# Kernel optimization log

Hardware: AMD Instinct MI355X
Metric: run time of the kernel (lower is better)

Reference implementation:

```python
import jax, jax.numpy as jnp
import numpy as np

B, L, D, F, T = 32, 768, 256, 256, 3072
_EPS = 1e-5


def _layernorm(h, g, b):
    mu = jnp.mean(h, axis=-1, keepdims=True)
    var = jnp.var(h, axis=-1, keepdims=True)
    return (h - mu) * jax.lax.rsqrt(var + _EPS) * g + b


def _conv1d(h, w, b):
    # h: [B, L, Cin], w: [K, Cin, Cout] (HIO), padding=1 matches torch Conv1d(padding=1)
    return jax.lax.conv_general_dilated(h, w, (1,), [(1, 1)], dimension_numbers=('NHC', 'HIO', 'NHC')) + b


def setup_inputs() -> dict:
    key = jax.random.key(0)
    ks = jax.random.split(key, 6)
    return {
        'x': jax.random.normal(ks[0], (B, L, D), jnp.float32),
        'target': jax.random.randint(ks[1], (B, L), 0, 4, jnp.int32),
        'mel_max_length': T,
        'conv1_w': jax.random.normal(ks[2], (3, D, F), jnp.float32) * 0.05,
        'conv1_b': jnp.zeros((F,), jnp.float32),
        'ln1_g': jnp.ones((F,), jnp.float32),
        'ln1_b': jnp.zeros((F,), jnp.float32),
        'conv2_w': jax.random.normal(ks[3], (3, F, F), jnp.float32) * 0.05,
        'conv2_b': jnp.zeros((F,), jnp.float32),
        'ln2_g': jnp.ones((F,), jnp.float32),
        'ln2_b': jnp.zeros((F,), jnp.float32),
        'lin_w': jax.random.normal(ks[4], (F, 1), jnp.float32) * 0.05,
        'lin_b': jnp.zeros((1,), jnp.float32),
    }


def reference(x, target, mel_max_length, conv1_w, conv1_b, ln1_g, ln1_b,
              conv2_w, conv2_b, ln2_g, ln2_b, lin_w, lin_b):
    alpha = 1.0
    # DurationPredictor: conv -> relu -> LN -> conv -> relu -> LN -> linear (dropout=0)
    h = _layernorm(jax.nn.relu(_conv1d(x, conv1_w, conv1_b)), ln1_g, ln1_b)
    h = _layernorm(jax.nn.relu(_conv1d(h, conv2_w, conv2_b)), ln2_g, ln2_b)
    dp_out = (h @ lin_w + lin_b)[..., 0]                       # [B, L]
    durations = jnp.exp(dp_out) * alpha                        # [B, L] float
    # Training branch: durations come from target
    dpo = jnp.round(target.astype(jnp.float32) * alpha).astype(jnp.int32)  # [B, L]
    # LR: alignment @ x realized as cumulative-duration searchsorted + gather
    cum = jnp.cumsum(dpo, axis=1)                              # [B, L]
    t = jnp.arange(mel_max_length, dtype=jnp.int32)            # [T]
    idx = jax.vmap(lambda c: jnp.searchsorted(c, t, side='right'))(cum)  # [B, T]
    mask = (t[None, :] < cum[:, -1:]).astype(x.dtype)          # [B, T] zero past total frames
    out = jnp.take_along_axis(x, jnp.clip(idx, 0, x.shape[1] - 1)[:, :, None], axis=1)
    out = out * mask[:, :, None]                               # [B, T, D]
    return (out, dpo, durations)
```

## Files before the change

### kernel.cpp

```cpp
#include <hip/hip_runtime.h>
#include <hip/hip_bf16.h>
#include <math.h>

#define BB 32
#define LL 768
#define DD 256
#define FF 256
#define TT 3072
#define MT 48
#define PAD 262
#define A1R 66

typedef __attribute__((ext_vector_type(8))) short bf16x8;
typedef __attribute__((ext_vector_type(4))) float f32x4;

__device__ inline unsigned short f2b(float f) {
    union { float f; unsigned u; } v; v.f = f;
    unsigned r = (v.u + 0x7FFF + ((v.u >> 16) & 1)) >> 16;
    return (unsigned short)r;
}

#define DPP_ROR_ADD(v, ctrl)                                                   \
    v += __int_as_float(__builtin_amdgcn_update_dpp(                           \
        0, __float_as_int(v), ctrl, 0xF, 0xF, false))

__device__ inline void red16_pair(float& a, float& b) {
    DPP_ROR_ADD(a, 0x128); DPP_ROR_ADD(b, 0x128);
    DPP_ROR_ADD(a, 0x124); DPP_ROR_ADD(b, 0x124);
    DPP_ROR_ADD(a, 0x122); DPP_ROR_ADD(b, 0x122);
    DPP_ROR_ADD(a, 0x121); DPP_ROR_ADD(b, 0x121);
}

__device__ inline float red16_one(float a) {
    DPP_ROR_ADD(a, 0x128);
    DPP_ROR_ADD(a, 0x124);
    DPP_ROR_ADD(a, 0x122);
    DPP_ROR_ADD(a, 0x121);
    return a;
}

__global__ __launch_bounds__(256) void prep_w_kernel(
    const float* __restrict__ w1, const float* __restrict__ w2,
    unsigned short* __restrict__ wQ1, unsigned short* __restrict__ wQ2)
{
    const int layer = blockIdx.x / 24;
    const int s  = blockIdx.x % 24;
    const int kc = s >> 3, c8 = s & 7;
    const float* __restrict__ w = layer ? w2 : w1;
    unsigned short* __restrict__ o = (layer ? wQ2 : wQ1) + s * 8192 + threadIdx.x * 32;
    const int n = threadIdx.x;

    alignas(16) unsigned short tmp[32];
#pragma unroll
    for (int q = 0; q < 4; ++q)
#pragma unroll
        for (int j = 0; j < 8; ++j) {
            const int cin = c8 * 32 + q * 8 + j;
            tmp[q * 8 + j] = f2b(w[((size_t)(kc * 256 + cin)) * 256 + n]);
        }
#pragma unroll
    for (int i = 0; i < 4; ++i)
        *reinterpret_cast<uint4*>(o + i * 8) = *reinterpret_cast<const uint4*>(tmp + i * 8);
}

__global__ __launch_bounds__(256) void fused_dp_kernel(
    const float* __restrict__ x,
    const unsigned short* __restrict__ wQ1,
    const unsigned short* __restrict__ wQ2,
    const float* __restrict__ c1b, const float* __restrict__ g1, const float* __restrict__ b1,
    const float* __restrict__ c2b, const float* __restrict__ g2, const float* __restrict__ b2,
    const float* __restrict__ lw,  const float* __restrict__ lb,
    float* __restrict__ out_dur)
{
    __shared__ union {
        unsigned short A1[A1R * PAD];
        unsigned short h2[50 * PAD];
    } sm;
    __shared__ float red[4][4][4][4][2];
    __shared__ float redp[4][3][4][4];
    __shared__ float fin[50][2];

    const int tid  = threadIdx.x;
    const int b    = blockIdx.x / (LL / MT);
    const int l0   = (blockIdx.x % (LL / MT)) * MT;
    const int wave = tid >> 6, lane = tid & 63;
    const int quad = lane >> 4, l16 = lane & 15;

    int   cols[4];
    float c1bv[4], g1v[4], b1v[4], c2bv[4], g2v[4], b2v[4], lwv[4];
#pragma unroll
    for (int nt = 0; nt < 4; ++nt) {
        const int c = wave * 64 + nt * 16 + l16;
        cols[nt] = c;
        c1bv[nt] = c1b[c]; g1v[nt] = g1[c]; b1v[nt] = b1[c];
        c2bv[nt] = c2b[c]; g2v[nt] = g2[c]; b2v[nt] = b2[c];
        lwv[nt]  = lw[c];
    }
    const float lbv = lb[0];

    {
        const int ch = (tid & 31) * 8;
        const int rr = tid >> 5;
        for (int p = 0; p < 9; ++p) {
            const int ar = p * 8 + rr;
            if (ar >= A1R) break;
            const int l = l0 - 2 + ar;
            bf16x8 val;
#pragma unroll
            for (int j = 0; j < 8; ++j) val[j] = 0;
            if (ar < 52 && l >= 0 && l < LL) {
                const float* pp = x + ((size_t)b * LL + l) * DD + ch;
                const float4 v0 = *reinterpret_cast<const float4*>(pp);
                const float4 v1 = *reinterpret_cast<const float4*>(pp + 4);
                val[0] = (short)f2b(v0.x); val[1] = (short)f2b(v0.y);
                val[2] = (short)f2b(v0.z); val[3] = (short)f2b(v0.w);
                val[4] = (short)f2b(v1.x); val[5] = (short)f2b(v1.y);
                val[6] = (short)f2b(v1.z); val[7] = (short)f2b(v1.w);
            }
            *reinterpret_cast<bf16x8*>(&sm.A1[ar * PAD + ch]) = val;
        }
    }
    __syncthreads();

    f32x4 acc1[4][4] = {};
    for (int s = 0; s < 24; ++s) {
        const int kc = s >> 3, c8 = s & 7;
        bf16x8 a[4], bf[4];
#pragma unroll
        for (int mt = 0; mt < 4; ++mt)
            a[mt] = *reinterpret_cast<const bf16x8*>(
                &sm.A1[(16 * mt + l16 + kc) * PAD + c8 * 32 + quad * 8]);
#pragma unroll
        for (int nt = 0; nt < 4; ++nt)
            bf[nt] = *reinterpret_cast<const bf16x8*>(
                wQ1 + (size_t)s * 8192 + cols[nt] * 32 + quad * 8);
#pragma unroll
        for (int mt = 0; mt < 4; ++mt)
#pragma unroll
            for (int nt = 0; nt < 4; ++nt)
                acc1[mt][nt] = __builtin_amdgcn_mfma_f32_16x16x32_bf16(
                    a[mt], bf[nt], acc1[mt][nt], 0, 0, 0);
    }
    __syncthreads();

#pragma unroll
    for (int mt = 0; mt < 4; ++mt)
#pragma unroll
        for (int r = 0; r < 4; ++r) {
            float s1 = 0.f, s2 = 0.f;
#pragma unroll
            for (int nt = 0; nt < 4; ++nt) {
                const float v = fmaxf(acc1[mt][nt][r] + c1bv[nt], 0.f);
                s1 += v; s2 += v * v;
            }
            red16_pair(s1, s2);
            if (l16 == 0) { red[wave][mt][quad][r][0] = s1; red[wave][mt][quad][r][1] = s2; }
        }
    __syncthreads();
    if (tid < 50) {
        const int mt = tid >> 4, q = (tid >> 2) & 3, r = tid & 3;
        const float s1 = red[0][mt][q][r][0] + red[1][mt][q][r][0]
                       + red[2][mt][q][r][0] + red[3][mt][q][r][0];
        const float s2 = red[0][mt][q][r][1] + red[1][mt][q][r][1]
                       + red[2][mt][q][r][1] + red[3][mt][q][r][1];
        const float mu  = s1 * (1.f / 256.f);
        const float var = s2 * (1.f / 256.f) - mu * mu;
        fin[tid][0] = mu;
        fin[tid][1] = rsqrtf(var + 1e-5f);
    }
    __syncthreads();

#pragma unroll
    for (int mt = 0; mt < 4; ++mt)
#pragma unroll
        for (int r = 0; r < 4; ++r) {
            const int rho = 16 * mt + quad * 4 + r;
            if (rho < 50) {
                const int gr = l0 - 1 + rho;
                const float mu = fin[rho][0], rstd = fin[rho][1];
#pragma unroll
                for (int nt = 0; nt < 4; ++nt) {
                    unsigned short hv = 0;
                    if (gr >= 0 && gr < LL) {
                        const float v = fmaxf(acc1[mt][nt][r] + c1bv[nt], 0.f);
                        hv = f2b((v - mu) * rstd * g1v[nt] + b1v[nt]);
                    }
                    sm.h2[rho * PAD + cols[nt]] = hv;
                }
            }
        }
    __syncthreads();

    f32x4 acc2[3][4] = {};
    for (int s = 0; s < 24; ++s) {
        const int kc = s >> 3, c8 = s & 7;
        bf16x8 a[3], bf[4];
#pragma unroll
        for (int mt = 0; mt < 3; ++mt)
            a[mt] = *reinterpret_cast<const bf16x8*>(
                &sm.h2[(16 * mt + l16 + kc) * PAD + c8 * 32 + quad * 8]);
#pragma unroll
        for (int nt = 0; nt < 4; ++nt)
            bf[nt] = *reinterpret_cast<const bf16x8*>(
                wQ2 + (size_t)s * 8192 + cols[nt] * 32 + quad * 8);
#pragma unroll
        for (int mt = 0; mt < 3; ++mt)
#pragma unroll
            for (int nt = 0; nt < 4; ++nt)
                acc2[mt][nt] = __builtin_amdgcn_mfma_f32_16x16x32_bf16(
                    a[mt], bf[nt], acc2[mt][nt], 0, 0, 0);
    }

#pragma unroll
    for (int mt = 0; mt < 3; ++mt)
#pragma unroll
        for (int r = 0; r < 4; ++r) {
            float s1 = 0.f, s2 = 0.f;
#pragma unroll
            for (int nt = 0; nt < 4; ++nt) {
                const float v = fmaxf(acc2[mt][nt][r] + c2bv[nt], 0.f);
                s1 += v; s2 += v * v;
            }
            red16_pair(s1, s2);
            if (l16 == 0) { red[wave][mt][quad][r][0] = s1; red[wave][mt][quad][r][1] = s2; }
        }
    __syncthreads();
    if (tid < MT) {
        const int mt = tid >> 4, q = (tid >> 2) & 3, r = tid & 3;
        const float s1 = red[0][mt][q][r][0] + red[1][mt][q][r][0]
                       + red[2][mt][q][r][0] + red[3][mt][q][r][0];
        const float s2 = red[0][mt][q][r][1] + red[1][mt][q][r][1]
                       + red[2][mt][q][r][1] + red[3][mt][q][r][1];
        const float mu  = s1 * (1.f / 256.f);
        const float var = s2 * (1.f / 256.f) - mu * mu;
        fin[tid][0] = mu;
        fin[tid][1] = rsqrtf(var + 1e-5f);
    }
    __syncthreads();

#pragma unroll
    for (int mt = 0; mt < 3; ++mt)
#pragma unroll
        for (int r = 0; r < 4; ++r) {
            const int rho = 16 * mt + quad * 4 + r;
            const float mu = fin[rho][0], rstd = fin[rho][1];
            float p = 0.f;
#pragma unroll
            for (int nt = 0; nt < 4; ++nt) {
                const float v = fmaxf(acc2[mt][nt][r] + c2bv[nt], 0.f);
                p += ((v - mu) * rstd * g2v[nt] + b2v[nt]) * lwv[nt];
            }
            p = red16_one(p);
            if (l16 == 0) redp[wave][mt][quad][r] = p;
        }
    __syncthreads();
    if (tid < MT) {
        const int mt = tid >> 4, q = (tid >> 2) & 3, r = tid & 3;
        const float dp = redp[0][mt][q][r] + redp[1][mt][q][r]
                       + redp[2][mt][q][r] + redp[3][mt][q][r] + lbv;
        out_dur[(size_t)b * LL + l0 + tid] = expf(dp);
    }
}

__global__ __launch_bounds__(256) void scan_kernel(
    const int* __restrict__ target,
    float* __restrict__ out_dpo,
    int* __restrict__ idx_map)
{
    __shared__ int tsum[256];
    const int b = blockIdx.x, tid = threadIdx.x;

    const int l = 3 * tid;
    const int v0 = target[b * LL + l];
    const int v1 = target[b * LL + l + 1];
    const int v2 = target[b * LL + l + 2];
    out_dpo[b * LL + l]     = (float)v0;
    out_dpo[b * LL + l + 1] = (float)v1;
    out_dpo[b * LL + l + 2] = (float)v2;

    const int s0 = v0, s1 = v0 + v1, s2 = v0 + v1 + v2;
    tsum[tid] = s2;
    __syncthreads();
    for (int off = 1; off < 256; off <<= 1) {
        int xq = (tid >= off) ? tsum[tid - off] : 0;
        __syncthreads();
        tsum[tid] += xq;
        __syncthreads();
    }
    const int excl = tsum[tid] - s2;

    for (int t = tid; t < TT; t += 256) idx_map[b * TT + t] = -1;
    __syncthreads();

    const int c0 = excl + s0, c1 = excl + s1, c2 = excl + s2;
    for (int t = excl; t < c0 && t < TT; ++t) idx_map[b * TT + t] = l;
    for (int t = c0;   t < c1 && t < TT; ++t) idx_map[b * TT + t] = l + 1;
    for (int t = c1;   t < c2 && t < TT; ++t) idx_map[b * TT + t] = l + 2;
}

__global__ __launch_bounds__(256) void gather_kernel(
    const float* __restrict__ x,
    const int* __restrict__ idx_map,
    float* __restrict__ out)
{
    const int wv = threadIdx.x >> 6, lane = threadIdx.x & 63;
    const int row = blockIdx.x * 4 + wv;
    const int b = row / TT, t = row - b * TT;
    const int idx = idx_map[b * TT + t];
    f32x4 val = {0.f, 0.f, 0.f, 0.f};
    if (idx >= 0)
        val = *reinterpret_cast<const f32x4*>(x + ((size_t)(b * LL + idx)) * DD + lane * 4);
    __builtin_nontemporal_store(val, reinterpret_cast<f32x4*>(out) + (size_t)row * (DD / 4) + lane);
}

extern "C" void kernel_launch(void* const* d_in, const int* in_sizes, int n_in,
                              void* d_out, int out_size, void* d_ws, size_t ws_size,
                              hipStream_t stream)
{
    const float* x      = (const float*)d_in[0];
    const int*   target = (const int*)  d_in[1];
    const float* c1w = (const float*)d_in[3];
    const float* c1b = (const float*)d_in[4];
    const float* g1  = (const float*)d_in[5];
    const float* b1  = (const float*)d_in[6];
    const float* c2w = (const float*)d_in[7];
    const float* c2b = (const float*)d_in[8];
    const float* g2  = (const float*)d_in[9];
    const float* b2  = (const float*)d_in[10];
    const float* lw  = (const float*)d_in[11];
    const float* lb  = (const float*)d_in[12];

    float* out0    = (float*)d_out;
    float* out_dpo = out0 + (size_t)BB * TT * DD;
    float* out_dur = out_dpo + (size_t)BB * LL;

    char* ws = (char*)d_ws;
    unsigned short* wQ1 = (unsigned short*)ws;                 ws += (size_t)24 * 8192 * 2;
    unsigned short* wQ2 = (unsigned short*)ws;                 ws += (size_t)24 * 8192 * 2;
    int* idx_map        = (int*)ws;

    prep_w_kernel<<<48, 256, 0, stream>>>(c1w, c2w, wQ1, wQ2);

    fused_dp_kernel<<<BB * (LL / MT), 256, 0, stream>>>(
        x, wQ1, wQ2, c1b, g1, b1, c2b, g2, b2, lw, lb, out_dur);

    scan_kernel<<<BB, 256, 0, stream>>>(target, out_dpo, idx_map);
    gather_kernel<<<BB * TT / 4, 256, 0, stream>>>(x, idx_map, out0);
}
```

Baseline: 199.4 us.

## Merge weight prep with scan kernel and widen fused conv block to 8 waves

```diff
diff --git a/kernel.cpp b/kernel.cpp
--- a/kernel.cpp
+++ b/kernel.cpp
@@ -39,31 +39,69 @@
     return a;
 }
 
-__global__ __launch_bounds__(256) void prep_w_kernel(
+__global__ __launch_bounds__(256) void prep_scan_kernel(
     const float* __restrict__ w1, const float* __restrict__ w2,
-    unsigned short* __restrict__ wQ1, unsigned short* __restrict__ wQ2)
+    unsigned short* __restrict__ wQ1, unsigned short* __restrict__ wQ2,
+    const int* __restrict__ target,
+    float* __restrict__ out_dpo,
+    int* __restrict__ idx_map)
 {
-    const int layer = blockIdx.x / 24;
-    const int s  = blockIdx.x % 24;
-    const int kc = s >> 3, c8 = s & 7;
-    const float* __restrict__ w = layer ? w2 : w1;
-    unsigned short* __restrict__ o = (layer ? wQ2 : wQ1) + s * 8192 + threadIdx.x * 32;
-    const int n = threadIdx.x;
-
-    alignas(16) unsigned short tmp[32];
-#pragma unroll
-    for (int q = 0; q < 4; ++q)
-#pragma unroll
-        for (int j = 0; j < 8; ++j) {
-            const int cin = c8 * 32 + q * 8 + j;
-            tmp[q * 8 + j] = f2b(w[((size_t)(kc * 256 + cin)) * 256 + n]);
-        }
-#pragma unroll
-    for (int i = 0; i < 4; ++i)
-        *reinterpret_cast<uint4*>(o + i * 8) = *reinterpret_cast<const uint4*>(tmp + i * 8);
-}
-
-__global__ __launch_bounds__(256) void fused_dp_kernel(
+    __shared__ int tsum[256];
+    const int tid = threadIdx.x;
+
+    if (blockIdx.x < 48) {
+        const int layer = blockIdx.x / 24;
+        const int s  = blockIdx.x % 24;
+        const int kc = s >> 3, c8 = s & 7;
+        const float* __restrict__ w = layer ? w2 : w1;
+        unsigned short* __restrict__ o = (layer ? wQ2 : wQ1) + s * 8192 + tid * 32;
+        const int n = tid;
+
+        alignas(16) unsigned short tmp[32];
+#pragma unroll
+        for (int q = 0; q < 4; ++q)
+#pragma unroll
+            for (int j = 0; j < 8; ++j) {
+                const int cin = c8 * 32 + q * 8 + j;
+                tmp[q * 8 + j] = f2b(w[((size_t)(kc * 256 + cin)) * 256 + n]);
+            }
+#pragma unroll
+        for (int i = 0; i < 4; ++i)
+            *reinterpret_cast<uint4*>(o + i * 8) = *reinterpret_cast<const uint4*>(tmp + i * 8);
+        return;
+    }
+
+    const int b = blockIdx.x - 48;
+
+    const int l = 3 * tid;
+    const int v0 = target[b * LL + l];
+    const int v1 = target[b * LL + l + 1];
+    const int v2 = target[b * LL + l + 2];
+    out_dpo[b * LL + l]     = (float)v0;
+    out_dpo[b * LL + l + 1] = (float)v1;
+    out_dpo[b * LL + l + 2] = (float)v2;
+
+    const int s0 = v0, s1 = v0 + v1, s2 = v0 + v1 + v2;
+    tsum[tid] = s2;
+    __syncthreads();
+    for (int off = 1; off < 256; off <<= 1) {
+        int xq = (tid >= off) ? tsum[tid - off] : 0;
+        __syncthreads();
+        tsum[tid] += xq;
+        __syncthreads();
+    }
+    const int excl = tsum[tid] - s2;
+
+    for (int t = tid; t < TT; t += 256) idx_map[b * TT + t] = -1;
+    __syncthreads();
+
+    const int c0 = excl + s0, c1 = excl + s1, c2 = excl + s2;
+    for (int t = excl; t < c0 && t < TT; ++t) idx_map[b * TT + t] = l;
+    for (int t = c0;   t < c1 && t < TT; ++t) idx_map[b * TT + t] = l + 1;
+    for (int t = c1;   t < c2 && t < TT; ++t) idx_map[b * TT + t] = l + 2;
+}
+
+__global__ __launch_bounds__(512, 4) void fused_dp_kernel(
     const float* __restrict__ x,
     const unsigned short* __restrict__ wQ1,
     const unsigned short* __restrict__ wQ2,
@@ -76,8 +114,8 @@
         unsigned short A1[A1R * PAD];
         unsigned short h2[50 * PAD];
     } sm;
-    __shared__ float red[4][4][4][4][2];
-    __shared__ float redp[4][3][4][4];
+    __shared__ float red[8][4][4][4][2];
+    __shared__ float redp[8][3][4][4];
     __shared__ float fin[50][2];
 
     const int tid  = threadIdx.x;
@@ -86,11 +124,11 @@
     const int wave = tid >> 6, lane = tid & 63;
     const int quad = lane >> 4, l16 = lane & 15;
 
-    int   cols[4];
-    float c1bv[4], g1v[4], b1v[4], c2bv[4], g2v[4], b2v[4], lwv[4];
-#pragma unroll
-    for (int nt = 0; nt < 4; ++nt) {
-        const int c = wave * 64 + nt * 16 + l16;
+    int   cols[2];
+    float c1bv[2], g1v[2], b1v[2], c2bv[2], g2v[2], b2v[2], lwv[2];
+#pragma unroll
+    for (int nt = 0; nt < 2; ++nt) {
+        const int c = wave * 32 + nt * 16 + l16;
         cols[nt] = c;
         c1bv[nt] = c1b[c]; g1v[nt] = g1[c]; b1v[nt] = b1[c];
         c2bv[nt] = c2b[c]; g2v[nt] = g2[c]; b2v[nt] = b2[c];
@@ -101,8 +139,8 @@
     {
         const int ch = (tid & 31) * 8;
         const int rr = tid >> 5;
-        for (int p = 0; p < 9; ++p) {
-            const int ar = p * 8 + rr;
+        for (int p = 0; p < 5; ++p) {
+            const int ar = p * 16 + rr;
             if (ar >= A1R) break;
             const int l = l0 - 2 + ar;
             bf16x8 val;
@@ -122,22 +160,22 @@
     }
     __syncthreads();
 
-    f32x4 acc1[4][4] = {};
+    f32x4 acc1[4][2] = {};
     for (int s = 0; s < 24; ++s) {
         const int kc = s >> 3, c8 = s & 7;
-        bf16x8 a[4], bf[4];
+        bf16x8 a[4], bf[2];
 #pragma unroll
         for (int mt = 0; mt < 4; ++mt)
             a[mt] = *reinterpret_cast<const bf16x8*>(
                 &sm.A1[(16 * mt + l16 + kc) * PAD + c8 * 32 + quad * 8]);
 #pragma unroll
-        for (int nt = 0; nt < 4; ++nt)
+        for (int nt = 0; nt < 2; ++nt)
             bf[nt] = *reinterpret_cast<const bf16x8*>(
                 wQ1 + (size_t)s * 8192 + cols[nt] * 32 + quad * 8);
 #pragma unroll
         for (int mt = 0; mt < 4; ++mt)
 #pragma unroll
-            for (int nt = 0; nt < 4; ++nt)
+            for (int nt = 0; nt < 2; ++nt)
                 acc1[mt][nt] = __builtin_amdgcn_mfma_f32_16x16x32_bf16(
                     a[mt], bf[nt], acc1[mt][nt], 0, 0, 0);
     }
@@ -149,7 +187,7 @@
         for (int r = 0; r < 4; ++r) {
             float s1 = 0.f, s2 = 0.f;
 #pragma unroll
-            for (int nt = 0; nt < 4; ++nt) {
+            for (int nt = 0; nt < 2; ++nt) {
                 const float v = fmaxf(acc1[mt][nt][r] + c1bv[nt], 0.f);
                 s1 += v; s2 += v * v;
             }
@@ -159,10 +197,9 @@
     __syncthreads();
     if (tid < 50) {
         const int mt = tid >> 4, q = (tid >> 2) & 3, r = tid & 3;
-        const float s1 = red[0][mt][q][r][0] + red[1][mt][q][r][0]
-                       + red[2][mt][q][r][0] + red[3][mt][q][r][0];
-        const float s2 = red[0][mt][q][r][1] + red[1][mt][q][r][1]
-                       + red[2][mt][q][r][1] + red[3][mt][q][r][1];
+        float s1 = 0.f, s2 = 0.f;
+#pragma unroll
+        for (int w = 0; w < 8; ++w) { s1 += red[w][mt][q][r][0]; s2 += red[w][mt][q][r][1]; }
         const float mu  = s1 * (1.f / 256.f);
         const float var = s2 * (1.f / 256.f) - mu * mu;
         fin[tid][0] = mu;
@@ -179,7 +216,7 @@
                 const int gr = l0 - 1 + rho;
                 const float mu = fin[rho][0], rstd = fin[rho][1];
 #pragma unroll
-                for (int nt = 0; nt < 4; ++nt) {
+                for (int nt = 0; nt < 2; ++nt) {
                     unsigned short hv = 0;
                     if (gr >= 0 && gr < LL) {
                         const float v = fmaxf(acc1[mt][nt][r] + c1bv[nt], 0.f);
@@ -191,22 +228,22 @@
         }
     __syncthreads();
 
-    f32x4 acc2[3][4] = {};
+    f32x4 acc2[3][2] = {};
     for (int s = 0; s < 24; ++s) {
         const int kc = s >> 3, c8 = s & 7;
-        bf16x8 a[3], bf[4];
+        bf16x8 a[3], bf[2];
 #pragma unroll
         for (int mt = 0; mt < 3; ++mt)
             a[mt] = *reinterpret_cast<const bf16x8*>(
                 &sm.h2[(16 * mt + l16 + kc) * PAD + c8 * 32 + quad * 8]);
 #pragma unroll
-        for (int nt = 0; nt < 4; ++nt)
+        for (int nt = 0; nt < 2; ++nt)
             bf[nt] = *reinterpret_cast<const bf16x8*>(
                 wQ2 + (size_t)s * 8192 + cols[nt] * 32 + quad * 8);
 #pragma unroll
         for (int mt = 0; mt < 3; ++mt)
 #pragma unroll
-            for (int nt = 0; nt < 4; ++nt)
+            for (int nt = 0; nt < 2; ++nt)
                 acc2[mt][nt] = __builtin_amdgcn_mfma_f32_16x16x32_bf16(
                     a[mt], bf[nt], acc2[mt][nt], 0, 0, 0);
     }
@@ -217,7 +254,7 @@
         for (int r = 0; r < 4; ++r) {
             float s1 = 0.f, s2 = 0.f;
 #pragma unroll
-            for (int nt = 0; nt < 4; ++nt) {
+            for (int nt = 0; nt < 2; ++nt) {
                 const float v = fmaxf(acc2[mt][nt][r] + c2bv[nt], 0.f);
                 s1 += v; s2 += v * v;
             }
@@ -227,10 +264,9 @@
     __syncthreads();
     if (tid < MT) {
         const int mt = tid >> 4, q = (tid >> 2) & 3, r = tid & 3;
-        const float s1 = red[0][mt][q][r][0] + red[1][mt][q][r][0]
-                       + red[2][mt][q][r][0] + red[3][mt][q][r][0];
-        const float s2 = red[0][mt][q][r][1] + red[1][mt][q][r][1]
-                       + red[2][mt][q][r][1] + red[3][mt][q][r][1];
+        float s1 = 0.f, s2 = 0.f;
+#pragma unroll
+        for (int w = 0; w < 8; ++w) { s1 += red[w][mt][q][r][0]; s2 += red[w][mt][q][r][1]; }
         const float mu  = s1 * (1.f / 256.f);
         const float var = s2 * (1.f / 256.f) - mu * mu;
         fin[tid][0] = mu;
@@ -246,7 +282,7 @@
             const float mu = fin[rho][0], rstd = fin[rho][1];
             float p = 0.f;
 #pragma unroll
-            for (int nt = 0; nt < 4; ++nt) {
+            for (int nt = 0; nt < 2; ++nt) {
                 const float v = fmaxf(acc2[mt][nt][r] + c2bv[nt], 0.f);
                 p += ((v - mu) * rstd * g2v[nt] + b2v[nt]) * lwv[nt];
             }
@@ -256,46 +292,11 @@
     __syncthreads();
     if (tid < MT) {
         const int mt = tid >> 4, q = (tid >> 2) & 3, r = tid & 3;
-        const float dp = redp[0][mt][q][r] + redp[1][mt][q][r]
-                       + redp[2][mt][q][r] + redp[3][mt][q][r] + lbv;
+        float dp = lbv;
+#pragma unroll
+        for (int w = 0; w < 8; ++w) dp += redp[w][mt][q][r];
         out_dur[(size_t)b * LL + l0 + tid] = expf(dp);
     }
-}
-
-__global__ __launch_bounds__(256) void scan_kernel(
-    const int* __restrict__ target,
-    float* __restrict__ out_dpo,
-    int* __restrict__ idx_map)
-{
-    __shared__ int tsum[256];
-    const int b = blockIdx.x, tid = threadIdx.x;
-
-    const int l = 3 * tid;
-    const int v0 = target[b * LL + l];
-    const int v1 = target[b * LL + l + 1];
-    const int v2 = target[b * LL + l + 2];
-    out_dpo[b * LL + l]     = (float)v0;
-    out_dpo[b * LL + l + 1] = (float)v1;
-    out_dpo[b * LL + l + 2] = (float)v2;
-
-    const int s0 = v0, s1 = v0 + v1, s2 = v0 + v1 + v2;
-    tsum[tid] = s2;
-    __syncthreads();
-    for (int off = 1; off < 256; off <<= 1) {
-        int xq = (tid >= off) ? tsum[tid - off] : 0;
-        __syncthreads();
-        tsum[tid] += xq;
-        __syncthreads();
-    }
-    const int excl = tsum[tid] - s2;
-
-    for (int t = tid; t < TT; t += 256) idx_map[b * TT + t] = -1;
-    __syncthreads();
-
-    const int c0 = excl + s0, c1 = excl + s1, c2 = excl + s2;
-    for (int t = excl; t < c0 && t < TT; ++t) idx_map[b * TT + t] = l;
-    for (int t = c0;   t < c1 && t < TT; ++t) idx_map[b * TT + t] = l + 1;
-    for (int t = c1;   t < c2 && t < TT; ++t) idx_map[b * TT + t] = l + 2;
 }
 
 __global__ __launch_bounds__(256) void gather_kernel(
@@ -339,11 +340,11 @@
     unsigned short* wQ2 = (unsigned short*)ws;                 ws += (size_t)24 * 8192 * 2;
     int* idx_map        = (int*)ws;
 
-    prep_w_kernel<<<48, 256, 0, stream>>>(c1w, c2w, wQ1, wQ2);
-
-    fused_dp_kernel<<<BB * (LL / MT), 256, 0, stream>>>(
+    prep_scan_kernel<<<48 + BB, 256, 0, stream>>>(
+        c1w, c2w, wQ1, wQ2, target, out_dpo, idx_map);
+
+    fused_dp_kernel<<<BB * (LL / MT), 512, 0, stream>>>(
         x, wQ1, wQ2, c1b, g1, b1, c2b, g2, b2, lw, lb, out_dur);
 
-    scan_kernel<<<BB, 256, 0, stream>>>(target, out_dpo, idx_map);
     gather_kernel<<<BB * TT / 4, 256, 0, stream>>>(x, idx_map, out0);
 }
```

Measured after the change: 231.5 us. 16.1% more time.
